# Kernel optimization log

Hardware: AMD Instinct MI355X
Metric: run time of the kernel (lower is better)

The kernel has to match this reference:

```python
import jax, jax.numpy as jnp
import numpy as np

N_NODES = 50000
N_EDGES = 800000
D_IN = 256
D_HID = 256
N_CLASSES = 40


def gcn_conv(x, W, b, src, dst, deg_inv_sqrt, n):
    # PyG GCNConv: linear transform first, then normalized scatter-add aggregation.
    x = x @ W                                   # [N, d_out]
    norm = deg_inv_sqrt[src] * deg_inv_sqrt[dst]  # [E+N] sym norm with self-loops
    msgs = x[src] * norm[:, None]               # gather source features
    out = jax.ops.segment_sum(msgs, dst, num_segments=n)
    return out + b


def setup_inputs() -> dict:
    key = jax.random.key(0)
    ks = jax.random.split(key, 6)
    x = jax.random.normal(ks[0], (N_NODES, D_IN), dtype=jnp.float32)
    edge_index = jax.random.randint(ks[1], (2, N_EDGES), 0, N_NODES, dtype=jnp.int64)
    s_in = 1.0 / np.sqrt(D_IN)
    s_h = 1.0 / np.sqrt(D_HID)
    W0 = jax.random.normal(ks[2], (D_IN, D_HID), dtype=jnp.float32) * s_in
    b0 = jnp.zeros((D_HID,), dtype=jnp.float32)
    W1 = jax.random.normal(ks[3], (D_HID, D_HID), dtype=jnp.float32) * s_h
    b1 = jnp.zeros((D_HID,), dtype=jnp.float32)
    W2 = jax.random.normal(ks[4], (D_HID, N_CLASSES), dtype=jnp.float32) * s_h
    b2 = jnp.zeros((N_CLASSES,), dtype=jnp.float32)
    return {"x": x, "edge_index": edge_index, "W0": W0, "b0": b0,
            "W1": W1, "b1": b1, "W2": W2, "b2": b2}


def reference(x, edge_index, W0, b0, W1, b1, W2, b2):
    n = x.shape[0]
    loops = jnp.arange(n, dtype=edge_index.dtype)
    src = jnp.concatenate([edge_index[0], loops])
    dst = jnp.concatenate([edge_index[1], loops])
    # degree (with self-loops) on destination nodes; deg >= 1 so rsqrt is safe
    deg = jax.ops.segment_sum(jnp.ones_like(dst, dtype=x.dtype), dst, num_segments=n)
    deg_inv_sqrt = jax.lax.rsqrt(deg)

    h = gcn_conv(x, W0, b0, src, dst, deg_inv_sqrt, n)
    h = jax.nn.relu(h)  # dropout is identity in eval mode
    h = gcn_conv(h, W1, b1, src, dst, deg_inv_sqrt, n)
    h = jax.nn.relu(h)
    h = gcn_conv(h, W2, b2, src, dst, deg_inv_sqrt, n)
    return jax.nn.log_softmax(h, axis=1)
```

## Files before the change

kernel.cpp:

```cpp
#include <hip/hip_runtime.h>
#include <hip/hip_bf16.h>
#include <cstdint>
#include <cstddef>


typedef unsigned char u8;
typedef unsigned short u16;
typedef unsigned int u32;
typedef __attribute__((ext_vector_type(8))) short bf16x8;
typedef __attribute__((ext_vector_type(4))) float f32x4;
typedef __attribute__((ext_vector_type(2))) float f32x2;

__device__ inline float bfl(u32 u) { return __uint_as_float(u << 16); }
__device__ inline float bfh(u32 u) { return __uint_as_float(u & 0xffff0000u); }
__device__ inline u16 f2bf(float f) {
  __hip_bfloat16 h = __float2bfloat16(f);
  return __builtin_bit_cast(u16, h);
}
__device__ inline u32 pk2bf(float lo, float hi) {
  return ((u32)f2bf(hi) << 16) | (u32)f2bf(lo);
}
__device__ inline u32 pk4fp8(float a, float b, float c, float d) {
  u32 w = __builtin_amdgcn_cvt_pk_fp8_f32(a, b, 0, false);
  w = __builtin_amdgcn_cvt_pk_fp8_f32(c, d, w, true);
  return w;
}
__device__ inline void up4fp8(u32 w, float* a) {
  f32x2 lo = __builtin_amdgcn_cvt_pk_f32_fp8(w, false);
  f32x2 hi = __builtin_amdgcn_cvt_pk_f32_fp8(w, true);
  a[0] += lo[0]; a[1] += lo[1]; a[2] += hi[0]; a[3] += hi[1];
}

__device__ inline void gl_lds16(const u16* g, u16* ldsbase) {
  __builtin_amdgcn_global_load_lds(
      (const __attribute__((address_space(1))) u32*)g,
      (__attribute__((address_space(3))) u32*)ldsbase, 16, 0, 0);
}

__global__ void k_prep(const float* __restrict__ W0, const float* __restrict__ W1,
                       const float* __restrict__ W2,
                       u16* __restrict__ Wt0, u16* __restrict__ Wt1,
                       u16* __restrict__ Wt2, int* __restrict__ cnt,
                       int* __restrict__ bflag,
                       u8* __restrict__ zu8, float* __restrict__ z40, int n) {
  const int t = blockIdx.x * 256 + threadIdx.x;
  if (t < 65536) {
    const int k = t >> 8, c = t & 255;
    Wt0[c * 256 + k] = f2bf(W0[t]);
    Wt1[c * 256 + k] = f2bf(W1[t]);
  } else if (t < 65536 + 16384) {
    const int t2 = t - 65536;
    const int k = t2 >> 6, nn = t2 & 63;
    const float v = (nn < 40) ? W2[k * 40 + nn] : 0.f;
    Wt2[nn * 256 + k] = f2bf(v);
  }
  const int u = t - (65536 + 16384);
  if (u >= 0) {
    if (u < n) cnt[u] = 0;
    if (u < 64) bflag[u] = 0;
    if (u < 256) zu8[u] = 0;
    if (u < 40) z40[u] = 0.f;
  }
}

__global__ void k_count(const int* __restrict__ dst, int* __restrict__ cnt,
                        int* __restrict__ rank, int E) {
  int e = blockIdx.x * blockDim.x + threadIdx.x;
  if (e < E) rank[e] = atomicAdd(&cnt[dst[e]], 1);
}

__global__ __launch_bounds__(1024) void k_scan(const int* __restrict__ cnt,
                                               int* __restrict__ rs,
                                               float* __restrict__ dis,
                                               int* __restrict__ bval,
                                               int* __restrict__ bpre,
                                               int* __restrict__ bflag, int n) {
  __shared__ int wsum[16];
  __shared__ int sbase;
  const int b = blockIdx.x;
  const int tid = threadIdx.x;
  const int lane = tid & 63, wid = tid >> 6;
  const int i = b * 1024 + tid;
  const int v = (i < n) ? cnt[i] : 0;
  int x = v;
#pragma unroll
  for (int off = 1; off < 64; off <<= 1) {
    int y = __shfl_up(x, off, 64);
    if (lane >= off) x += y;
  }
  if (lane == 63) wsum[wid] = x;
  __syncthreads();
  if (wid == 0) {
    int w = (lane < 16) ? wsum[lane] : 0;
#pragma unroll
    for (int off = 1; off < 16; off <<= 1) {
      int y = __shfl_up(w, off, 64);
      if (lane >= off) w += y;
    }
    if (lane < 16) wsum[lane] = w;
  }
  __syncthreads();
  const int total = wsum[15];
  const int excl = (wid > 0 ? wsum[wid - 1] : 0) + (x - v);

  if (tid == 0) {
    if (b == 0) {
      atomicExch(&bpre[0], total);
      __threadfence();
      atomicExch(&bflag[0], 2);
      sbase = 0;
    } else {
      atomicExch(&bval[b], total);
      __threadfence();
      atomicExch(&bflag[b], 1);
      int run = 0, j = b - 1;
      while (true) {
        int f;
        while ((f = atomicAdd(&bflag[j], 0)) == 0) {}
        if (f == 2) { run += atomicAdd(&bpre[j], 0); break; }
        run += atomicAdd(&bval[j], 0);
        --j;
      }
      atomicExch(&bpre[b], run + total);
      __threadfence();
      atomicExch(&bflag[b], 2);
      sbase = run;
    }
  }
  __syncthreads();
  const int base = sbase;
  if (i < n) {
    rs[i] = base + excl;
    dis[i] = rsqrtf((float)(1 + v));
  }
  if (b == (int)gridDim.x - 1 && tid == 0) rs[n] = base + total;
}

__global__ void k_fill(const int* __restrict__ src, const int* __restrict__ dst,
                       const int* __restrict__ rank, const int* __restrict__ rs,
                       int* __restrict__ csr, int E) {
  int e = blockIdx.x * blockDim.x + threadIdx.x;
  if (e < E) csr[rs[dst[e]] + rank[e]] = src[e];
}

template <bool F32A>
__global__ __launch_bounds__(256) void k_gemm256(const void* __restrict__ Aptr,
                                                 const u16* __restrict__ Wt,
                                                 const float* __restrict__ dis,
                                                 u8* __restrict__ C, int M) {
  __shared__ u16 As[128 * 64];
  __shared__ u16 Bs[128 * 64];
  const int tid = threadIdx.x;
  const int wid = tid >> 6, lane = tid & 63;
  const int wave_m = wid >> 1, wave_n = wid & 1;
  const int m0 = blockIdx.x * 128, n0 = blockIdx.y * 128;
  const int quad = lane >> 4, col = lane & 15;

  const int srl = lane >> 3;
  const int sseg = lane & 7;

  const int ra = wave_m * 64 + col;
  const int rb = wave_n * 64 + col;

  f32x4 acc[4][4];
#pragma unroll
  for (int i = 0; i < 4; ++i)
#pragma unroll
    for (int j = 0; j < 4; ++j) acc[i][j] = (f32x4){0.f, 0.f, 0.f, 0.f};

  for (int k0 = 0; k0 < 256; k0 += 64) {
#pragma unroll
    for (int blk = 0; blk < 4; ++blk) {
      const int R = wid * 32 + blk * 8;
      const int r = R + srl;
      const int q = (sseg - r) & 7;
      if (F32A) {
        const float* A = (const float*)Aptr;
        const int gm = m0 + r;
        float4 lo = make_float4(0.f, 0.f, 0.f, 0.f), hi = lo;
        if (gm < M) {
          lo = *(const float4*)(A + (size_t)gm * 256 + k0 + q * 8);
          hi = *(const float4*)(A + (size_t)gm * 256 + k0 + q * 8 + 4);
        }
        uint4 w;
        w.x = pk2bf(lo.x, lo.y); w.y = pk2bf(lo.z, lo.w);
        w.z = pk2bf(hi.x, hi.y); w.w = pk2bf(hi.z, hi.w);
        *(uint4*)&As[r * 64 + sseg * 8] = w;
      } else {
        const u16* A = (const u16*)Aptr;
        if (m0 + r < M)
          gl_lds16(A + (size_t)(m0 + r) * 256 + k0 + q * 8, &As[R * 64]);
      }
      gl_lds16(Wt + (size_t)(n0 + r) * 256 + k0 + q * 8, &Bs[R * 64]);
    }
    __syncthreads();

#pragma unroll
    for (int kk = 0; kk < 2; ++kk) {
      bf16x8 af[4], bf[4];
#pragma unroll
      for (int i = 0; i < 4; ++i) {
        const int r = ra + i * 16;
        af[i] = *(const bf16x8*)&As[r * 64 + ((quad + kk * 4 + r) & 7) * 8];
      }
#pragma unroll
      for (int j = 0; j < 4; ++j) {
        const int r = rb + j * 16;
        bf[j] = *(const bf16x8*)&Bs[r * 64 + ((quad + kk * 4 + r) & 7) * 8];
      }
#pragma unroll
      for (int i = 0; i < 4; ++i)
#pragma unroll
        for (int j = 0; j < 4; ++j)
          acc[i][j] = __builtin_amdgcn_mfma_f32_16x16x32_bf16(bf[j], af[i], acc[i][j], 0, 0, 0);
    }
    __syncthreads();
  }

#pragma unroll
  for (int i = 0; i < 4; ++i) {
    const int m = m0 + wave_m * 64 + i * 16 + col;
    if (m < M) {
      const float dd = dis[m];
#pragma unroll
      for (int j = 0; j < 4; ++j) {
        const int n = n0 + wave_n * 64 + j * 16 + quad * 4;
        const u32 w = pk4fp8(acc[i][j][0] * dd, acc[i][j][1] * dd,
                             acc[i][j][2] * dd, acc[i][j][3] * dd);
        *(u32*)(C + (size_t)m * 256 + n) = w;
      }
    }
  }
}

__global__ __launch_bounds__(256) void k_agg256(const u8* __restrict__ u,
                                                const int* __restrict__ rs,
                                                const int* __restrict__ csr,
                                                const float* __restrict__ dis,
                                                const float* __restrict__ b,
                                                u16* __restrict__ out, int n) {
  const int wid = threadIdx.x >> 6, lane = threadIdx.x & 63;
  const int d = blockIdx.x * 4 + wid;
  if (d >= n) return;
  const int q = lane >> 4, sl = lane & 15;
  const int cb = sl * 16;
  float a[16] = {0.f, 0.f, 0.f, 0.f, 0.f, 0.f, 0.f, 0.f,
                 0.f, 0.f, 0.f, 0.f, 0.f, 0.f, 0.f, 0.f};
  {
    const int sidx = q ? n : d;
    const uint4 v = *(const uint4*)(u + (size_t)sidx * 256 + cb);
    up4fp8(v.x, a); up4fp8(v.y, a + 4); up4fp8(v.z, a + 8); up4fp8(v.w, a + 12);
  }
  const int p1 = rs[d + 1];
  for (int p = rs[d]; p < p1; p += 16) {
    int idx[4];
#pragma unroll
    for (int i = 0; i < 4; ++i) {
      const int e = p + 4 * i + q;
      idx[i] = (e < p1) ? csr[e] : n;
    }
    uint4 v[4];
#pragma unroll
    for (int i = 0; i < 4; ++i)
      v[i] = *(const uint4*)(u + (size_t)idx[i] * 256 + cb);
#pragma unroll
    for (int i = 0; i < 4; ++i) {
      up4fp8(v[i].x, a); up4fp8(v[i].y, a + 4);
      up4fp8(v[i].z, a + 8); up4fp8(v[i].w, a + 12);
    }
  }
#pragma unroll
  for (int j = 0; j < 16; ++j) {
    a[j] += __shfl_xor(a[j], 16, 64);
    a[j] += __shfl_xor(a[j], 32, 64);
  }
  if (q == 0) {
    const float dd = dis[d];
    uint4 o0, o1;
    const float4 b0 = *(const float4*)(b + cb);
    const float4 b1 = *(const float4*)(b + cb + 4);
    const float4 b2 = *(const float4*)(b + cb + 8);
    const float4 b3 = *(const float4*)(b + cb + 12);
    o0.x = pk2bf(fmaxf(dd * a[0] + b0.x, 0.f), fmaxf(dd * a[1] + b0.y, 0.f));
    o0.y = pk2bf(fmaxf(dd * a[2] + b0.z, 0.f), fmaxf(dd * a[3] + b0.w, 0.f));
    o0.z = pk2bf(fmaxf(dd * a[4] + b1.x, 0.f), fmaxf(dd * a[5] + b1.y, 0.f));
    o0.w = pk2bf(fmaxf(dd * a[6] + b1.z, 0.f), fmaxf(dd * a[7] + b1.w, 0.f));
    o1.x = pk2bf(fmaxf(dd * a[8] + b2.x, 0.f), fmaxf(dd * a[9] + b2.y, 0.f));
    o1.y = pk2bf(fmaxf(dd * a[10] + b2.z, 0.f), fmaxf(dd * a[11] + b2.w, 0.f));
    o1.z = pk2bf(fmaxf(dd * a[12] + b3.x, 0.f), fmaxf(dd * a[13] + b3.y, 0.f));
    o1.w = pk2bf(fmaxf(dd * a[14] + b3.z, 0.f), fmaxf(dd * a[15] + b3.w, 0.f));
    *(uint4*)(out + (size_t)d * 256 + cb) = o0;
    *(uint4*)(out + (size_t)d * 256 + cb + 8) = o1;
  }
}

__global__ __launch_bounds__(256) void k_gemm40(const u16* __restrict__ A,
                                                const u16* __restrict__ Wt2,
                                                const float* __restrict__ dis,
                                                float* __restrict__ C, int M) {
  const int wv = threadIdx.x >> 6, lane = threadIdx.x & 63;
  const int quad = lane >> 4, col = lane & 15;
  const int m0 = blockIdx.x * 128 + wv * 32;
  f32x4 acc[2][3];
#pragma unroll
  for (int i = 0; i < 2; ++i)
#pragma unroll
    for (int j = 0; j < 3; ++j) acc[i][j] = (f32x4){0.f, 0.f, 0.f, 0.f};
  for (int k0 = 0; k0 < 256; k0 += 32) {
    bf16x8 af[2], bf[3];
#pragma unroll
    for (int i = 0; i < 2; ++i) {
      int row = m0 + i * 16 + col;
      row = (row < M) ? row : (M - 1);
      af[i] = *(const bf16x8*)(A + (size_t)row * 256 + k0 + quad * 8);
    }
#pragma unroll
    for (int j = 0; j < 3; ++j)
      bf[j] = *(const bf16x8*)(Wt2 + (size_t)(j * 16 + col) * 256 + k0 + quad * 8);
#pragma unroll
    for (int i = 0; i < 2; ++i)
#pragma unroll
      for (int j = 0; j < 3; ++j)
        acc[i][j] = __builtin_amdgcn_mfma_f32_16x16x32_bf16(bf[j], af[i], acc[i][j], 0, 0, 0);
  }
#pragma unroll
  for (int i = 0; i < 2; ++i) {
    const int m = m0 + i * 16 + col;
    if (m < M) {
      const float dd = dis[m];
#pragma unroll
      for (int j = 0; j < 3; ++j) {
        const int nn = j * 16 + quad * 4;
        if (nn < 40) {
          float4 o = make_float4(acc[i][j][0] * dd, acc[i][j][1] * dd,
                                 acc[i][j][2] * dd, acc[i][j][3] * dd);
          *(float4*)(C + (size_t)m * 40 + nn) = o;
        }
      }
    }
  }
}

__global__ __launch_bounds__(256) void k_agg40(const float* __restrict__ u,
                                               const int* __restrict__ rs,
                                               const int* __restrict__ csr,
                                               const float* __restrict__ dis,
                                               const float* __restrict__ b,
                                               float* __restrict__ out, int n) {
  const int wid = threadIdx.x >> 6, lane = threadIdx.x & 63;
  const int d = blockIdx.x * 4 + wid;
  if (d >= n) return;
  const int slot = lane / 20;
  const int sl = lane % 20;
  const bool act = slot < 3;
  const int col = sl * 2;
  float a0 = 0.f, a1 = 0.f;
  if (slot == 0) {
    const float2 v = *(const float2*)(u + (size_t)d * 40 + col);
    a0 = v.x; a1 = v.y;
  }
  const int p1 = rs[d + 1];
  for (int p = rs[d]; p < p1; p += 12) {
    int idx[4];
#pragma unroll
    for (int i = 0; i < 4; ++i) {
      const int e = p + 3 * i + slot;
      idx[i] = (act && e < p1) ? csr[e] : n;
    }
    float2 v[4];
#pragma unroll
    for (int i = 0; i < 4; ++i)
      v[i] = *(const float2*)(u + (size_t)idx[i] * 40 + col);
#pragma unroll
    for (int i = 0; i < 4; ++i) { a0 += v[i].x; a1 += v[i].y; }
  }
  a0 += __shfl(a0, lane + 20, 64) + __shfl(a0, lane + 40, 64);
  a1 += __shfl(a1, lane + 20, 64) + __shfl(a1, lane + 40, 64);
  float l0 = -INFINITY, l1 = -INFINITY;
  if (lane < 20) {
    const float dd = dis[d];
    l0 = dd * a0 + b[col];
    l1 = dd * a1 + b[col + 1];
  }
  float mx = fmaxf(l0, l1);
#pragma unroll
  for (int off = 16; off; off >>= 1) mx = fmaxf(mx, __shfl_xor(mx, off, 32));
  float e0 = (lane < 20) ? expf(l0 - mx) : 0.f;
  float e1 = (lane < 20) ? expf(l1 - mx) : 0.f;
  float sm = e0 + e1;
#pragma unroll
  for (int off = 16; off; off >>= 1) sm += __shfl_xor(sm, off, 32);
  if (lane < 20) {
    const float ls = mx + logf(sm);
    float2 o = make_float2(l0 - ls, l1 - ls);
    *(float2*)(out + (size_t)d * 40 + col) = o;
  }
}

extern "C" void kernel_launch(void* const* d_in, const int* in_sizes, int n_in,
                              void* d_out, int out_size, void* d_ws, size_t ws_size,
                              hipStream_t stream) {
  const float* x  = (const float*)d_in[0];
  const int*   ei = (const int*)d_in[1];
  const float* W0 = (const float*)d_in[2];
  const float* b0 = (const float*)d_in[3];
  const float* W1 = (const float*)d_in[4];
  const float* b1 = (const float*)d_in[5];
  const float* W2 = (const float*)d_in[6];
  const float* b2 = (const float*)d_in[7];
  float* out = (float*)d_out;

  const int N = in_sizes[0] / 256;
  const int E = in_sizes[1] / 2;
  const int* src = ei;
  const int* dst = ei + E;

  char* p = (char*)d_ws;
  auto carve = [&](size_t bytes) {
    char* q = p;
    p += (bytes + 255) & ~(size_t)255;
    return q;
  };
  u8*    uf8   = (u8*)carve((size_t)(N + 1) * 256);
  u16*   h     = (u16*)carve((size_t)N * 256 * 2);
  float* u40   = (float*)carve((size_t)(N + 1) * 40 * 4);
  u16*   Wt0   = (u16*)carve(256 * 256 * 2);
  u16*   Wt1   = (u16*)carve(256 * 256 * 2);
  u16*   Wt2   = (u16*)carve(64 * 256 * 2);
  float* dis   = (float*)carve((size_t)N * 4);
  int*   cnt   = (int*)carve((size_t)N * 4);
  int*   rs    = (int*)carve((size_t)(N + 1) * 4);
  int*   rank  = (int*)carve((size_t)E * 4);
  int*   csr   = (int*)carve((size_t)(E + 16) * 4);
  int*   bval  = (int*)carve(64 * 4);
  int*   bpre  = (int*)carve(64 * 4);
  int*   bflag = (int*)carve(64 * 4);

  const int prep_items = 65536 + 16384 + N;
  k_prep<<<(prep_items + 255) / 256, 256, 0, stream>>>(
      W0, W1, W2, Wt0, Wt1, Wt2, cnt, bflag,
      uf8 + (size_t)N * 256, u40 + (size_t)N * 40, N);

  const int eb = (E + 255) / 256;
  const int nb = (N + 1023) / 1024;
  k_count<<<eb, 256, 0, stream>>>(dst, cnt, rank, E);
  k_scan<<<nb, 1024, 0, stream>>>(cnt, rs, dis, bval, bpre, bflag, N);
  k_fill<<<eb, 256, 0, stream>>>(src, dst, rank, rs, csr, E);

  const dim3 ggrid((N + 127) / 128, 2);
  const int agrid = (N + 3) / 4;

  k_gemm256<true><<<ggrid, 256, 0, stream>>>(x, Wt0, dis, uf8, N);
  k_agg256<<<agrid, 256, 0, stream>>>(uf8, rs, csr, dis, b0, h, N);
  k_gemm256<false><<<ggrid, 256, 0, stream>>>(h, Wt1, dis, uf8, N);
  k_agg256<<<agrid, 256, 0, stream>>>(uf8, rs, csr, dis, b1, h, N);
  k_gemm40<<<(N + 127) / 128, 256, 0, stream>>>(h, Wt2, dis, u40, N);
  k_agg40<<<agrid, 256, 0, stream>>>(u40, rs, csr, dis, b2, out, N);
}
```

Measured before the change: 326.3 us.

## Merge prep/count and fill/gemm0 kernels; split aggregation launches in halves

Folds the edge counting into the weight-prep kernel and the CSR fill into the first GEMM kernel, with block-index ranges picking the role, so fewer kernels launch and independent work shares one grid. Counter zeroing moves to a hipMemsetAsync. Each 256-wide aggregation is now split into two launches over node halves, which adds launches for unclear benefit. Two things need checking: the fill blocks and GEMM blocks share a kernel that reserves 32KB of LDS, and the GEMM reads dis written by the scan, which runs before it, so that ordering is safe.

```diff
diff --git a/kernel.cpp b/kernel.cpp
--- a/kernel.cpp
+++ b/kernel.cpp
@@ -37,13 +37,21 @@
       (__attribute__((address_space(3))) u32*)ldsbase, 16, 0, 0);
 }
 
-__global__ void k_prep(const float* __restrict__ W0, const float* __restrict__ W1,
-                       const float* __restrict__ W2,
-                       u16* __restrict__ Wt0, u16* __restrict__ Wt1,
-                       u16* __restrict__ Wt2, int* __restrict__ cnt,
-                       int* __restrict__ bflag,
-                       u8* __restrict__ zu8, float* __restrict__ z40, int n) {
-  const int t = blockIdx.x * 256 + threadIdx.x;
+__global__ void k_prepcount(const int* __restrict__ dst, int* __restrict__ cnt,
+                            int* __restrict__ rank, int E, int CB,
+                            const float* __restrict__ W0,
+                            const float* __restrict__ W1,
+                            const float* __restrict__ W2,
+                            u16* __restrict__ Wt0, u16* __restrict__ Wt1,
+                            u16* __restrict__ Wt2, int* __restrict__ bflag,
+                            u8* __restrict__ zu8, float* __restrict__ z40,
+                            int n) {
+  if ((int)blockIdx.x < CB) {
+    const int e = blockIdx.x * 256 + threadIdx.x;
+    if (e < E) rank[e] = atomicAdd(&cnt[dst[e]], 1);
+    return;
+  }
+  const int t = (blockIdx.x - CB) * 256 + threadIdx.x;
   if (t < 65536) {
     const int k = t >> 8, c = t & 255;
     Wt0[c * 256 + k] = f2bf(W0[t]);
@@ -56,17 +64,10 @@
   }
   const int u = t - (65536 + 16384);
   if (u >= 0) {
-    if (u < n) cnt[u] = 0;
     if (u < 64) bflag[u] = 0;
     if (u < 256) zu8[u] = 0;
     if (u < 40) z40[u] = 0.f;
   }
-}
-
-__global__ void k_count(const int* __restrict__ dst, int* __restrict__ cnt,
-                        int* __restrict__ rank, int E) {
-  int e = blockIdx.x * blockDim.x + threadIdx.x;
-  if (e < E) rank[e] = atomicAdd(&cnt[dst[e]], 1);
 }
 
 __global__ __launch_bounds__(1024) void k_scan(const int* __restrict__ cnt,
@@ -136,24 +137,16 @@
   if (b == (int)gridDim.x - 1 && tid == 0) rs[n] = base + total;
 }
 
-__global__ void k_fill(const int* __restrict__ src, const int* __restrict__ dst,
-                       const int* __restrict__ rank, const int* __restrict__ rs,
-                       int* __restrict__ csr, int E) {
-  int e = blockIdx.x * blockDim.x + threadIdx.x;
-  if (e < E) csr[rs[dst[e]] + rank[e]] = src[e];
-}
-
 template <bool F32A>
-__global__ __launch_bounds__(256) void k_gemm256(const void* __restrict__ Aptr,
-                                                 const u16* __restrict__ Wt,
-                                                 const float* __restrict__ dis,
-                                                 u8* __restrict__ C, int M) {
-  __shared__ u16 As[128 * 64];
-  __shared__ u16 Bs[128 * 64];
+__device__ inline void gemm256_block(const void* __restrict__ Aptr,
+                                     const u16* __restrict__ Wt,
+                                     const float* __restrict__ dis,
+                                     u8* __restrict__ C, int M,
+                                     int bx, int by, u16* As, u16* Bs) {
   const int tid = threadIdx.x;
   const int wid = tid >> 6, lane = tid & 63;
   const int wave_m = wid >> 1, wave_n = wid & 1;
-  const int m0 = blockIdx.x * 128, n0 = blockIdx.y * 128;
+  const int m0 = bx * 128, n0 = by * 128;
   const int quad = lane >> 4, col = lane & 15;
 
   const int srl = lane >> 3;
@@ -233,15 +226,42 @@
   }
 }
 
+__global__ __launch_bounds__(256) void k_gemmfill(
+    const float* __restrict__ x, const u16* __restrict__ Wt0,
+    const float* __restrict__ dis, u8* __restrict__ C, int M,
+    const int* __restrict__ src, const int* __restrict__ dst,
+    const int* __restrict__ rank, const int* __restrict__ rs,
+    int* __restrict__ csr, int E, int FB) {
+  __shared__ u16 As[128 * 64];
+  __shared__ u16 Bs[128 * 64];
+  if ((int)blockIdx.x < FB) {
+    const int e = blockIdx.x * 256 + threadIdx.x;
+    if (e < E) csr[rs[dst[e]] + rank[e]] = src[e];
+    return;
+  }
+  const int bb = blockIdx.x - FB;
+  gemm256_block<true>(x, Wt0, dis, C, M, bb >> 1, bb & 1, As, Bs);
+}
+
+__global__ __launch_bounds__(256) void k_gemm256(const u16* __restrict__ A,
+                                                 const u16* __restrict__ Wt,
+                                                 const float* __restrict__ dis,
+                                                 u8* __restrict__ C, int M) {
+  __shared__ u16 As[128 * 64];
+  __shared__ u16 Bs[128 * 64];
+  gemm256_block<false>(A, Wt, dis, C, M, blockIdx.x, blockIdx.y, As, Bs);
+}
+
 __global__ __launch_bounds__(256) void k_agg256(const u8* __restrict__ u,
                                                 const int* __restrict__ rs,
                                                 const int* __restrict__ csr,
                                                 const float* __restrict__ dis,
                                                 const float* __restrict__ b,
-                                                u16* __restrict__ out, int n) {
+                                                u16* __restrict__ out, int n,
+                                                int d0, int d1) {
   const int wid = threadIdx.x >> 6, lane = threadIdx.x & 63;
-  const int d = blockIdx.x * 4 + wid;
-  if (d >= n) return;
+  const int d = d0 + blockIdx.x * 4 + wid;
+  if (d >= d1) return;
   const int q = lane >> 4, sl = lane & 15;
   const int cb = sl * 16;
   float a[16] = {0.f, 0.f, 0.f, 0.f, 0.f, 0.f, 0.f, 0.f,
@@ -436,24 +456,30 @@
   int*   bpre  = (int*)carve(64 * 4);
   int*   bflag = (int*)carve(64 * 4);
 
-  const int prep_items = 65536 + 16384 + N;
-  k_prep<<<(prep_items + 255) / 256, 256, 0, stream>>>(
-      W0, W1, W2, Wt0, Wt1, Wt2, cnt, bflag,
-      uf8 + (size_t)N * 256, u40 + (size_t)N * 40, N);
-
-  const int eb = (E + 255) / 256;
+  const int CB = (E + 255) / 256;
+  const int prep_items = 65536 + 16384 + 256;
+  const int PB = (prep_items + 255) / 256;
   const int nb = (N + 1023) / 1024;
-  k_count<<<eb, 256, 0, stream>>>(dst, cnt, rank, E);
+  const int GB = ((N + 127) / 128) * 2;
+
+  hipMemsetAsync(cnt, 0, (size_t)N * 4, stream);
+
+  k_prepcount<<<CB + PB, 256, 0, stream>>>(dst, cnt, rank, E, CB,
+                                           W0, W1, W2, Wt0, Wt1, Wt2, bflag,
+                                           uf8 + (size_t)N * 256,
+                                           u40 + (size_t)N * 40, N);
   k_scan<<<nb, 1024, 0, stream>>>(cnt, rs, dis, bval, bpre, bflag, N);
-  k_fill<<<eb, 256, 0, stream>>>(src, dst, rank, rs, csr, E);
-
-  const dim3 ggrid((N + 127) / 128, 2);
-  const int agrid = (N + 3) / 4;
-
-  k_gemm256<true><<<ggrid, 256, 0, stream>>>(x, Wt0, dis, uf8, N);
-  k_agg256<<<agrid, 256, 0, stream>>>(uf8, rs, csr, dis, b0, h, N);
-  k_gemm256<false><<<ggrid, 256, 0, stream>>>(h, Wt1, dis, uf8, N);
-  k_agg256<<<agrid, 256, 0, stream>>>(uf8, rs, csr, dis, b1, h, N);
+  k_gemmfill<<<CB + GB, 256, 0, stream>>>(x, Wt0, dis, uf8, N,
+                                          src, dst, rank, rs, csr, E, CB);
+
+  const int Nh = N / 2;
+  const int ga1 = (Nh + 3) / 4, ga2 = (N - Nh + 3) / 4;
+
+  k_agg256<<<ga1, 256, 0, stream>>>(uf8, rs, csr, dis, b0, h, N, 0, Nh);
+  k_agg256<<<ga2, 256, 0, stream>>>(uf8, rs, csr, dis, b0, h, N, Nh, N);
+  k_gemm256<<<dim3((N + 127) / 128, 2), 256, 0, stream>>>(h, Wt1, dis, uf8, N);
+  k_agg256<<<ga1, 256, 0, stream>>>(uf8, rs, csr, dis, b1, h, N, 0, Nh);
+  k_agg256<<<ga2, 256, 0, stream>>>(uf8, rs, csr, dis, b1, h, N, Nh, N);
   k_gemm40<<<(N + 127) / 128, 256, 0, stream>>>(h, Wt2, dis, u40, N);
-  k_agg40<<<agrid, 256, 0, stream>>>(u40, rs, csr, dis, b2, out, N);
-}
+  k_agg40<<<(N + 3) / 4, 256, 0, stream>>>(u40, rs, csr, dis, b2, out, N);
+}
```

After: 334.8 us. 1.03x slower.

## Stage full-K A tile in LDS once and read W fragments from global

Applied to the files above, without the earlier changes.

The GEMM kernel now loads the entire 128x256 A tile into LDS (64 KB) in one pass with an XOR-style swizzle, then runs all K steps without intermediate barriers. B (weight) fragments are read straight from global or L2 instead of being staged in LDS. The h buffer is padded by 128 rows so the unguarded bf16 loads past M stay in bounds. This removes per-K-step syncs and B staging, but the larger LDS footprint lowers occupancy and the uncoalesced weight loads depend on cache hits.

```diff
diff --git a/kernel.cpp b/kernel.cpp
--- a/kernel.cpp
+++ b/kernel.cpp
@@ -148,73 +148,66 @@
                                                  const u16* __restrict__ Wt,
                                                  const float* __restrict__ dis,
                                                  u8* __restrict__ C, int M) {
-  __shared__ u16 As[128 * 64];
-  __shared__ u16 Bs[128 * 64];
+  __shared__ u16 As[128 * 256];
   const int tid = threadIdx.x;
   const int wid = tid >> 6, lane = tid & 63;
   const int wave_m = wid >> 1, wave_n = wid & 1;
   const int m0 = blockIdx.x * 128, n0 = blockIdx.y * 128;
   const int quad = lane >> 4, col = lane & 15;
 
-  const int srl = lane >> 3;
-  const int sseg = lane & 7;
-
-  const int ra = wave_m * 64 + col;
-  const int rb = wave_n * 64 + col;
-
-  f32x4 acc[4][4];
-#pragma unroll
-  for (int i = 0; i < 4; ++i)
-#pragma unroll
-    for (int j = 0; j < 4; ++j) acc[i][j] = (f32x4){0.f, 0.f, 0.f, 0.f};
-
-  for (int k0 = 0; k0 < 256; k0 += 64) {
-#pragma unroll
-    for (int blk = 0; blk < 4; ++blk) {
-      const int R = wid * 32 + blk * 8;
-      const int r = R + srl;
-      const int q = (sseg - r) & 7;
+  {
+    const int slot = lane & 31;
+    const int rh = lane >> 5;
+    const int R0 = wid * 32;
+#pragma unroll
+    for (int i = 0; i < 16; ++i) {
+      const int row = R0 + 2 * i + rh;
+      const int g = (slot - 2 * (row & 15)) & 31;
       if (F32A) {
         const float* A = (const float*)Aptr;
-        const int gm = m0 + r;
+        const int gm = m0 + row;
         float4 lo = make_float4(0.f, 0.f, 0.f, 0.f), hi = lo;
         if (gm < M) {
-          lo = *(const float4*)(A + (size_t)gm * 256 + k0 + q * 8);
-          hi = *(const float4*)(A + (size_t)gm * 256 + k0 + q * 8 + 4);
+          lo = *(const float4*)(A + (size_t)gm * 256 + g * 8);
+          hi = *(const float4*)(A + (size_t)gm * 256 + g * 8 + 4);
         }
         uint4 w;
         w.x = pk2bf(lo.x, lo.y); w.y = pk2bf(lo.z, lo.w);
         w.z = pk2bf(hi.x, hi.y); w.w = pk2bf(hi.z, hi.w);
-        *(uint4*)&As[r * 64 + sseg * 8] = w;
+        *(uint4*)&As[row * 256 + slot * 8] = w;
       } else {
         const u16* A = (const u16*)Aptr;
-        if (m0 + r < M)
-          gl_lds16(A + (size_t)(m0 + r) * 256 + k0 + q * 8, &As[R * 64]);
+        gl_lds16(A + (size_t)(m0 + row) * 256 + g * 8, &As[(R0 + 2 * i) * 256]);
       }
-      gl_lds16(Wt + (size_t)(n0 + r) * 256 + k0 + q * 8, &Bs[R * 64]);
-    }
-    __syncthreads();
-
-#pragma unroll
-    for (int kk = 0; kk < 2; ++kk) {
-      bf16x8 af[4], bf[4];
-#pragma unroll
-      for (int i = 0; i < 4; ++i) {
-        const int r = ra + i * 16;
-        af[i] = *(const bf16x8*)&As[r * 64 + ((quad + kk * 4 + r) & 7) * 8];
-      }
-#pragma unroll
-      for (int j = 0; j < 4; ++j) {
-        const int r = rb + j * 16;
-        bf[j] = *(const bf16x8*)&Bs[r * 64 + ((quad + kk * 4 + r) & 7) * 8];
-      }
-#pragma unroll
-      for (int i = 0; i < 4; ++i)
-#pragma unroll
-        for (int j = 0; j < 4; ++j)
-          acc[i][j] = __builtin_amdgcn_mfma_f32_16x16x32_bf16(bf[j], af[i], acc[i][j], 0, 0, 0);
-    }
-    __syncthreads();
+    }
+  }
+  __syncthreads();
+
+  f32x4 acc[4][4];
+#pragma unroll
+  for (int i = 0; i < 4; ++i)
+#pragma unroll
+    for (int j = 0; j < 4; ++j) acc[i][j] = (f32x4){0.f, 0.f, 0.f, 0.f};
+
+#pragma unroll
+  for (int k0 = 0; k0 < 256; k0 += 32) {
+    const int ks = (k0 >> 3) + quad;
+    bf16x8 af[4], bf[4];
+#pragma unroll
+    for (int j = 0; j < 4; ++j) {
+      const int nr = n0 + wave_n * 64 + j * 16 + col;
+      bf[j] = *(const bf16x8*)(Wt + (size_t)nr * 256 + k0 + quad * 8);
+    }
+#pragma unroll
+    for (int i = 0; i < 4; ++i) {
+      const int r = wave_m * 64 + i * 16 + col;
+      af[i] = *(const bf16x8*)&As[r * 256 + ((ks + 2 * col) & 31) * 8];
+    }
+#pragma unroll
+    for (int i = 0; i < 4; ++i)
+#pragma unroll
+      for (int j = 0; j < 4; ++j)
+        acc[i][j] = __builtin_amdgcn_mfma_f32_16x16x32_bf16(bf[j], af[i], acc[i][j], 0, 0, 0);
   }
 
 #pragma unroll
@@ -422,7 +415,7 @@
     return q;
   };
   u8*    uf8   = (u8*)carve((size_t)(N + 1) * 256);
-  u16*   h     = (u16*)carve((size_t)N * 256 * 2);
+  u16*   h     = (u16*)carve((size_t)(N + 128) * 256 * 2);
   float* u40   = (float*)carve((size_t)(N + 1) * 40 * 4);
   u16*   Wt0   = (u16*)carve(256 * 256 * 2);
   u16*   Wt1   = (u16*)carve(256 * 256 * 2);
```

Measured after the change: 340.5 us. 1.04x slower.
